# Optimization experiments

Hardware: AMD Instinct MI355X
Metric: run time of the kernel (lower is better)

Reference implementation:

```python
import jax, jax.numpy as jnp
import numpy as np

K = 128           # top-k
NUM_SAMPLES = 500 # perturbation samples
SIGMA = 0.05      # noise scale (forward arg sigma in the torch module)


def setup_inputs() -> dict:
    key = jax.random.key(0)
    k1, k2 = jax.random.split(key)
    x = jax.random.normal(k1, (32, 2048), dtype=jnp.float32)
    noise = jax.random.normal(k2, (32, NUM_SAMPLES, 2048), dtype=jnp.float32)
    return {"x": x, "noise": noise}


def reference(x, noise):
    # x: (b, d) scores; noise: (b, n, d) standard-normal perturbations.
    b, d = x.shape
    n = noise.shape[1]
    perturbed = x[:, None, :] + noise * SIGMA          # (b, n, d)
    _, idx = jax.lax.top_k(perturbed, K)               # (b, n, K) indices into d
    idx = jnp.sort(idx, axis=-1)                       # sorted, matching torch.sort
    # indicators[b,j,d] = mean_n one_hot(idx[b,n,j], d)
    # Computed with a scatter-add instead of materializing the (b,n,K,d) one-hot.
    bi = jnp.arange(b)[:, None, None]                  # (b,1,1)
    ki = jnp.arange(K)[None, None, :]                  # (1,1,K)
    counts = jnp.zeros((b, K, d), dtype=x.dtype).at[bi, ki, idx].add(1.0)
    indicators = counts / n                            # (b, K, d)
    return indicators, idx
```

## Files before the change

kernel.cpp:

```cpp
#include <hip/hip_runtime.h>


constexpr int B_     = 32;
constexpr int D_     = 2048;
constexpr int NS_    = 500;
constexpr int TOPK_  = 128;
constexpr int SLACK_ = 32;
constexpr float SIGMA_  = 0.05f;
constexpr int PER_LANE_ = D_ / 64;
constexpr int HALF_  = D_ / 2;
constexpr int HPL_   = HALF_ / 64;
constexpr int CAP_   = 256;
constexpr int SLOTS_ = CAP_ / 64;
constexpr int JCHUNK_ = 8;

__device__ __forceinline__ uint32_t order_key(float f) {
  uint32_t u = __float_as_uint(f);
  return (u & 0x80000000u) ? ~u : (u | 0x80000000u);
}
__device__ __forceinline__ float inv_key(uint32_t k) {
  uint32_t u = (k & 0x80000000u) ? (k & 0x7FFFFFFFu) : ~k;
  return __uint_as_float(u);
}

__global__ __launch_bounds__(64) void ptk_cutoff(const float* __restrict__ x,
                                                 float* __restrict__ cutf) {
  const int lane = threadIdx.x & 63;
  const int b = blockIdx.x;
  const float* __restrict__ xr = x + (size_t)b * D_;
  uint32_t keys[PER_LANE_];
#pragma unroll
  for (int j = 0; j < PER_LANE_; j += 4) {
    const float4 xv = *reinterpret_cast<const float4*>(xr + lane * PER_LANE_ + j);
    keys[j + 0] = order_key(xv.x); keys[j + 1] = order_key(xv.y);
    keys[j + 2] = order_key(xv.z); keys[j + 3] = order_key(xv.w);
  }
  uint32_t prefix = 0; int k = TOPK_ + SLACK_;
#pragma unroll 1
  for (int bit = 31; bit >= 0; --bit) {
    const uint32_t want = (prefix >> bit) | 1u;
    int c = 0;
#pragma unroll
    for (int j = 0; j < PER_LANE_; ++j) c += ((keys[j] >> bit) == want) ? 1 : 0;
#pragma unroll
    for (int off = 32; off >= 1; off >>= 1) c += __shfl_xor(c, off);
    if (c >= k) prefix |= (1u << bit); else k -= c;
  }
  if (lane == 0) cutf[b] = inv_key(prefix);
}

__global__ __launch_bounds__(256) void ptk_select(
    const float* __restrict__ x, const float* __restrict__ noise,
    const float* __restrict__ cutf, float* __restrict__ out_idx) {
  __shared__ uint2 comp[2][2 * CAP_];
  __shared__ int cnts[2][2];

  const int lane = threadIdx.x & 63;
  const int wave = threadIdx.x >> 6;
  const int pair = wave >> 1;
  const int half = wave & 1;
  const int row  = blockIdx.x * 2 + pair;
  const int b = row / NS_;

  const float* __restrict__ xr = x + (size_t)b * D_ + half * HALF_;
  const float* __restrict__ nr = noise + (size_t)row * D_ + half * HALF_;
  const int base_l = lane * HPL_;
  const int base_i = half * HALF_ + base_l;

  float p[HPL_];
#pragma unroll
  for (int j = 0; j < HPL_; j += 4) {
    const float4 nv = *reinterpret_cast<const float4*>(nr + base_l + j);
    const float4 xv = *reinterpret_cast<const float4*>(xr + base_l + j);
    p[j + 0] = fmaf(SIGMA_, nv.x, xv.x);
    p[j + 1] = fmaf(SIGMA_, nv.y, xv.y);
    p[j + 2] = fmaf(SIGMA_, nv.z, xv.z);
    p[j + 3] = fmaf(SIGMA_, nv.w, xv.w);
  }

  const float cf = cutf[b];

  uint32_t m = 0;
#pragma unroll
  for (int j = 0; j < HPL_; ++j) m |= (p[j] >= cf) ? (1u << j) : 0u;
  const int cnt = __popc(m);

  const uint64_t below = (lane == 0) ? 0ull : ((~0ull) >> (64 - lane));
  int offset = 0, Cw = 0;
#pragma unroll
  for (int t = 0; t < 5; ++t) {
    const uint64_t mb = __ballot((cnt >> t) & 1);
    offset += (int)__popcll(mb & below) << t;
    Cw     += (int)__popcll(mb) << t;
  }
  if (lane == 0) cnts[pair][half] = Cw;

  {
    uint32_t mm = m; int q = half * CAP_ + offset;
    while (mm) {
      const int j = __ffs(mm) - 1; mm &= mm - 1;
      comp[pair][q] = make_uint2(order_key(p[j]), (uint32_t)(base_i + j));
      ++q;
    }
  }
  __syncthreads();

  if (half) return;

  const int C0 = cnts[pair][0];
  const int C1 = cnts[pair][1];
  const int C  = C0 + C1;

  float* __restrict__ idx_row = out_idx + (size_t)row * TOPK_;

  if (C >= TOPK_ && C <= CAP_) {
    uint32_t kk[SLOTS_], ki[SLOTS_];
    bool valid[SLOTS_];
#pragma unroll
    for (int s = 0; s < SLOTS_; ++s) {
      const int q = (s << 6) + lane;
      const int a = (q < C0) ? q : (CAP_ + q - C0);
      valid[s] = (q < C);
      const uint2 v = valid[s] ? comp[pair][a] : make_uint2(0u, 0u);
      kk[s] = v.x; ki[s] = v.y;
    }

    uint32_t orv = 0u, andv = 0xFFFFFFFFu;
#pragma unroll
    for (int s = 0; s < SLOTS_; ++s) {
      orv  |= valid[s] ? kk[s] : 0u;
      andv &= valid[s] ? kk[s] : 0xFFFFFFFFu;
    }
#pragma unroll
    for (int off = 32; off >= 1; off >>= 1) {
      orv  |= __shfl_xor(orv, off);
      andv &= __shfl_xor(andv, off);
    }
    const uint32_t diff = orv ^ andv;

    uint32_t prefix; int r;
    if (diff == 0u) {
      prefix = orv; r = TOPK_;
    } else {
      const int startbit = 31 - __clz(diff);
      prefix = (startbit == 31) ? 0u : (andv & (0xFFFFFFFFu << (startbit + 1)));
      int k = TOPK_;
      int A = C;
#pragma unroll 1
      for (int bit = startbit; bit >= 0; --bit) {
        const uint32_t want = (prefix >> bit) | 1u;
        int c = 0;
#pragma unroll
        for (int s = 0; s < SLOTS_; ++s)
          c += __popcll(__ballot((kk[s] >> bit) == want));
        if (c >= k) { prefix |= (1u << bit); A = c; }
        else        { k -= c; A -= c; }
        if (A == 1) {
          uint32_t mykey = 0u; bool have = false;
#pragma unroll
          for (int s = 0; s < SLOTS_; ++s) {
            const bool hit = valid[s] && ((kk[s] >> bit) == (prefix >> bit));
            mykey = hit ? kk[s] : mykey;
            have |= hit;
          }
          const uint64_t mb = __ballot(have);
          const int src = __ffsll((unsigned long long)mb) - 1;
          prefix = __shfl(mykey, src);
          k = 1;
          break;
        }
      }
      r = k;
    }

    int sel_run = 0, eq_run = 0;
#pragma unroll
    for (int s = 0; s < SLOTS_; ++s) {
      const bool gt = kk[s] > prefix;
      const bool eq = kk[s] == prefix;
      const uint64_t meq = __ballot(eq);
      const int eqrank = eq_run + __popcll(meq & below);
      const bool sel = gt || (eq && (eqrank < r));
      const uint64_t msel = __ballot(sel);
      if (sel) {
        const int pos = sel_run + __popcll(msel & below);
        idx_row[pos] = (float)(int)ki[s];
      }
      sel_run += __popcll(msel);
      eq_run  += __popcll(meq);
    }
  } else {
    const float* __restrict__ xr2 = x + (size_t)b * D_;
    const float* __restrict__ nr2 = noise + (size_t)row * D_;
    const int bi = lane * PER_LANE_;
    uint32_t keys[PER_LANE_];
#pragma unroll
    for (int j = 0; j < PER_LANE_; ++j)
      keys[j] = order_key(fmaf(SIGMA_, nr2[bi + j], xr2[bi + j]));

    uint32_t prefix = 0; int k = TOPK_;
#pragma unroll 1
    for (int bit = 31; bit >= 0; --bit) {
      const uint32_t want = (prefix >> bit) | 1u;
      int c = 0;
#pragma unroll
      for (int j = 0; j < PER_LANE_; ++j) c += ((keys[j] >> bit) == want) ? 1 : 0;
#pragma unroll
      for (int off = 32; off >= 1; off >>= 1) c += __shfl_xor(c, off);
      if (c >= k) prefix |= (1u << bit); else k -= c;
    }
    const int r = k;

    int gt = 0, eq = 0;
#pragma unroll
    for (int j = 0; j < PER_LANE_; ++j) {
      gt += (keys[j] > prefix) ? 1 : 0;
      eq += (keys[j] == prefix) ? 1 : 0;
    }
    uint32_t incl2 = (uint32_t)gt | ((uint32_t)eq << 16);
#pragma unroll
    for (int off = 1; off < 64; off <<= 1) {
      uint32_t y = __shfl_up(incl2, (unsigned)off);
      if (lane >= off) incl2 += y;
    }
    const int gt_base = (int)(incl2 & 0xFFFFu) - gt;
    const int eq_base = (int)(incl2 >> 16) - eq;
    int pos = gt_base + min(eq_base, r);
    int eq_seen = eq_base;
#pragma unroll
    for (int j = 0; j < PER_LANE_; ++j) {
      const uint32_t kj = keys[j];
      bool s = false;
      if (kj > prefix) s = true;
      else if (kj == prefix) { s = (eq_seen < r); eq_seen++; }
      if (s) { idx_row[pos] = (float)(bi + j); pos++; }
    }
  }
}

__global__ __launch_bounds__(256) void ptk_hist(
    const float* __restrict__ out_idx, float* __restrict__ indicators) {
  __shared__ int hist[JCHUNK_][D_];

  const int tid   = threadIdx.x;
  const int b     = blockIdx.x >> 4;
  const int chunk = blockIdx.x & 15;
  const int j0    = chunk * JCHUNK_;

  int4* h4 = (int4*)hist;
  for (int t = tid; t < JCHUNK_ * D_ / 4; t += 256)
    h4[t] = make_int4(0, 0, 0, 0);
  __syncthreads();

  const float* __restrict__ src = out_idx + (size_t)b * NS_ * TOPK_ + j0;
  for (int t = tid; t < NS_ * 2; t += 256) {
    const int n = t >> 1;
    const int q = (t & 1) << 2;
    const float4 v = *reinterpret_cast<const float4*>(src + (size_t)n * TOPK_ + q);
    atomicAdd(&hist[q + 0][(int)v.x], 1);
    atomicAdd(&hist[q + 1][(int)v.y], 1);
    atomicAdd(&hist[q + 2][(int)v.z], 1);
    atomicAdd(&hist[q + 3][(int)v.w], 1);
  }
  __syncthreads();

  float4* __restrict__ dst =
      (float4*)(indicators + ((size_t)b * TOPK_ + j0) * D_);
  for (int t = tid; t < JCHUNK_ * D_ / 4; t += 256) {
    const int4 h = h4[t];
    float4 o;
    o.x = (float)h.x / (float)NS_;
    o.y = (float)h.y / (float)NS_;
    o.z = (float)h.z / (float)NS_;
    o.w = (float)h.w / (float)NS_;
    dst[t] = o;
  }
}

extern "C" void kernel_launch(void* const* d_in, const int* in_sizes, int n_in,
                              void* d_out, int out_size, void* d_ws, size_t ws_size,
                              hipStream_t stream) {
  const float* x     = (const float*)d_in[0];
  const float* noise = (const float*)d_in[1];
  float* indicators  = (float*)d_out;
  float* out_idx     = (float*)d_out + (size_t)B_ * TOPK_ * D_;
  float* cutf        = (float*)d_ws;

  hipLaunchKernelGGL(ptk_cutoff, dim3(B_), dim3(64), 0, stream, x, cutf);

  const int rows = B_ * NS_;
  hipLaunchKernelGGL(ptk_select, dim3(rows / 2), dim3(256), 0, stream,
                     x, noise, cutf, out_idx);

  hipLaunchKernelGGL(ptk_hist, dim3(B_ * 16), dim3(256), 0, stream,
                     out_idx, indicators);
}
```

Before: 224.1 us.

## Split each select row across four waves and halve histogram j-chunk

The select kernel now gives each row a full 256-thread block, with the four waves each filtering a quarter of the row into their own compaction segment. Before, two waves shared a row and each block handled two rows. Candidate writes are clamped per wave, and wave 0 merges the four segments by prefix offsets. The histogram kernel uses 4 top-k positions per block instead of 8, which doubles the block count and lowers LDS per block. This is meant to shorten the serial compaction per wave and raise occupancy and parallelism, at the cost of more idle waves during the merge and more blocks launched.

```diff
diff --git a/kernel.cpp b/kernel.cpp
--- a/kernel.cpp
+++ b/kernel.cpp
@@ -8,11 +8,11 @@
 constexpr int SLACK_ = 32;
 constexpr float SIGMA_  = 0.05f;
 constexpr int PER_LANE_ = D_ / 64;
-constexpr int HALF_  = D_ / 2;
-constexpr int HPL_   = HALF_ / 64;
+constexpr int QTR_   = D_ / 4;
+constexpr int QPL_   = QTR_ / 64;
 constexpr int CAP_   = 256;
 constexpr int SLOTS_ = CAP_ / 64;
-constexpr int JCHUNK_ = 8;
+constexpr int JCHUNK_ = 4;
 
 __device__ __forceinline__ uint32_t order_key(float f) {
   uint32_t u = __float_as_uint(f);
@@ -52,24 +52,22 @@
 __global__ __launch_bounds__(256) void ptk_select(
     const float* __restrict__ x, const float* __restrict__ noise,
     const float* __restrict__ cutf, float* __restrict__ out_idx) {
-  __shared__ uint2 comp[2][2 * CAP_];
-  __shared__ int cnts[2][2];
+  __shared__ uint2 comp[4 * CAP_];
+  __shared__ int cnts[4];
 
   const int lane = threadIdx.x & 63;
   const int wave = threadIdx.x >> 6;
-  const int pair = wave >> 1;
-  const int half = wave & 1;
-  const int row  = blockIdx.x * 2 + pair;
+  const int row  = blockIdx.x;
   const int b = row / NS_;
 
-  const float* __restrict__ xr = x + (size_t)b * D_ + half * HALF_;
-  const float* __restrict__ nr = noise + (size_t)row * D_ + half * HALF_;
-  const int base_l = lane * HPL_;
-  const int base_i = half * HALF_ + base_l;
-
-  float p[HPL_];
-#pragma unroll
-  for (int j = 0; j < HPL_; j += 4) {
+  const float* __restrict__ xr = x + (size_t)b * D_ + wave * QTR_;
+  const float* __restrict__ nr = noise + (size_t)row * D_ + wave * QTR_;
+  const int base_l = lane * QPL_;
+  const int base_i = wave * QTR_ + base_l;
+
+  float p[QPL_];
+#pragma unroll
+  for (int j = 0; j < QPL_; j += 4) {
     const float4 nv = *reinterpret_cast<const float4*>(nr + base_l + j);
     const float4 xv = *reinterpret_cast<const float4*>(xr + base_l + j);
     p[j + 0] = fmaf(SIGMA_, nv.x, xv.x);
@@ -82,34 +80,36 @@
 
   uint32_t m = 0;
 #pragma unroll
-  for (int j = 0; j < HPL_; ++j) m |= (p[j] >= cf) ? (1u << j) : 0u;
+  for (int j = 0; j < QPL_; ++j) m |= (p[j] >= cf) ? (1u << j) : 0u;
   const int cnt = __popc(m);
 
   const uint64_t below = (lane == 0) ? 0ull : ((~0ull) >> (64 - lane));
   int offset = 0, Cw = 0;
 #pragma unroll
-  for (int t = 0; t < 5; ++t) {
+  for (int t = 0; t < 4; ++t) {
     const uint64_t mb = __ballot((cnt >> t) & 1);
     offset += (int)__popcll(mb & below) << t;
     Cw     += (int)__popcll(mb) << t;
   }
-  if (lane == 0) cnts[pair][half] = Cw;
+  if (lane == 0) cnts[wave] = Cw;
 
   {
-    uint32_t mm = m; int q = half * CAP_ + offset;
+    uint32_t mm = m; int q = offset;
     while (mm) {
       const int j = __ffs(mm) - 1; mm &= mm - 1;
-      comp[pair][q] = make_uint2(order_key(p[j]), (uint32_t)(base_i + j));
+      if (q < CAP_)
+        comp[wave * CAP_ + q] = make_uint2(order_key(p[j]),
+                                           (uint32_t)(base_i + j));
       ++q;
     }
   }
   __syncthreads();
 
-  if (half) return;
-
-  const int C0 = cnts[pair][0];
-  const int C1 = cnts[pair][1];
-  const int C  = C0 + C1;
+  if (wave) return;
+
+  const int C0 = cnts[0], C1 = cnts[1], C2 = cnts[2], C3 = cnts[3];
+  const int s1 = C0, s2 = C0 + C1, s3 = C0 + C1 + C2;
+  const int C  = s3 + C3;
 
   float* __restrict__ idx_row = out_idx + (size_t)row * TOPK_;
 
@@ -119,9 +119,13 @@
 #pragma unroll
     for (int s = 0; s < SLOTS_; ++s) {
       const int q = (s << 6) + lane;
-      const int a = (q < C0) ? q : (CAP_ + q - C0);
+      int a;
+      if (q < s1)      a = q;
+      else if (q < s2) a = CAP_     + (q - s1);
+      else if (q < s3) a = 2 * CAP_ + (q - s2);
+      else             a = 3 * CAP_ + (q - s3);
       valid[s] = (q < C);
-      const uint2 v = valid[s] ? comp[pair][a] : make_uint2(0u, 0u);
+      const uint2 v = valid[s] ? comp[a] : make_uint2(0u, 0u);
       kk[s] = v.x; ki[s] = v.y;
     }
 
@@ -243,8 +247,8 @@
   __shared__ int hist[JCHUNK_][D_];
 
   const int tid   = threadIdx.x;
-  const int b     = blockIdx.x >> 4;
-  const int chunk = blockIdx.x & 15;
+  const int b     = blockIdx.x >> 5;
+  const int chunk = blockIdx.x & 31;
   const int j0    = chunk * JCHUNK_;
 
   int4* h4 = (int4*)hist;
@@ -253,14 +257,12 @@
   __syncthreads();
 
   const float* __restrict__ src = out_idx + (size_t)b * NS_ * TOPK_ + j0;
-  for (int t = tid; t < NS_ * 2; t += 256) {
-    const int n = t >> 1;
-    const int q = (t & 1) << 2;
-    const float4 v = *reinterpret_cast<const float4*>(src + (size_t)n * TOPK_ + q);
-    atomicAdd(&hist[q + 0][(int)v.x], 1);
-    atomicAdd(&hist[q + 1][(int)v.y], 1);
-    atomicAdd(&hist[q + 2][(int)v.z], 1);
-    atomicAdd(&hist[q + 3][(int)v.w], 1);
+  for (int n = tid; n < NS_; n += 256) {
+    const float4 v = *reinterpret_cast<const float4*>(src + (size_t)n * TOPK_);
+    atomicAdd(&hist[0][(int)v.x], 1);
+    atomicAdd(&hist[1][(int)v.y], 1);
+    atomicAdd(&hist[2][(int)v.z], 1);
+    atomicAdd(&hist[3][(int)v.w], 1);
   }
   __syncthreads();
 
@@ -289,9 +291,9 @@
   hipLaunchKernelGGL(ptk_cutoff, dim3(B_), dim3(64), 0, stream, x, cutf);
 
   const int rows = B_ * NS_;
-  hipLaunchKernelGGL(ptk_select, dim3(rows / 2), dim3(256), 0, stream,
+  hipLaunchKernelGGL(ptk_select, dim3(rows), dim3(256), 0, stream,
                      x, noise, cutf, out_idx);
 
-  hipLaunchKernelGGL(ptk_hist, dim3(B_ * 16), dim3(256), 0, stream,
-                     out_idx, indicators);
-}
+  hipLaunchKernelGGL(ptk_hist, dim3(B_ * (TOPK_ / JCHUNK_)), dim3(256), 0,
+                     stream, out_idx, indicators);
+}
```

Result: no change. 227.6 us (+1.6%).
